# Kernel tuning notes

Hardware: AMD Instinct MI355X
Metric: run time of the kernel (lower is better)

The kernel has to match this reference:

```python
import jax, jax.numpy as jnp
import numpy as np

B, C, OUT, K, H, W = 16, 128, 128, 3, 128, 128
EPS = 1e-5


def setup_inputs() -> dict:
    key = jax.random.key(0)
    ks = jax.random.split(key, 16)
    s = 0.05  # weight init scale to keep activations tame
    d = {
        "ir_feat": jax.random.normal(ks[0], (B, C, H, W), jnp.float32),
        "vi_feat": jax.random.normal(ks[1], (B, C, H, W), jnp.float32),
        # kernel_gen: 1x1 convs on pooled [B,2C,1,1] -> matmuls
        "kg_w1": jax.random.normal(ks[2], (C // 2, 2 * C), jnp.float32) * s,
        "kg_b1": jax.random.normal(ks[3], (C // 2,), jnp.float32) * s,
        "kg_w2": jax.random.normal(ks[4], (OUT * C * K * K, C // 2), jnp.float32) * s,
        "kg_b2": jax.random.normal(ks[5], (OUT * C * K * K,), jnp.float32) * s,
        # bias_gen
        "bg_w1": jax.random.normal(ks[6], (C // 4, 2 * C), jnp.float32) * s,
        "bg_b1": jax.random.normal(ks[7], (C // 4,), jnp.float32) * s,
        "bg_w2": jax.random.normal(ks[8], (OUT, C // 4), jnp.float32) * s,
        "bg_b2": jax.random.normal(ks[9], (OUT,), jnp.float32) * s,
        # enhance: 1x1 conv (no bias) + BN (eval-mode running stats)
        "en_w": jax.random.normal(ks[10], (C, 2 * C), jnp.float32) * s,
        "bn_gamma": jnp.ones((C,), jnp.float32),
        "bn_beta": jnp.zeros((C,), jnp.float32),
        "bn_mean": jax.random.normal(ks[11], (C,), jnp.float32) * 0.1,
        "bn_var": jax.random.uniform(ks[12], (C,), jnp.float32, 0.5, 1.5),
    }
    return d


def reference(ir_feat, vi_feat, kg_w1, kg_b1, kg_w2, kg_b2,
              bg_w1, bg_b1, bg_w2, bg_b2, en_w,
              bn_gamma, bn_beta, bn_mean, bn_var):
    concat = jnp.concatenate([ir_feat, vi_feat], axis=1)        # [B,2C,H,W]
    pooled = concat.mean(axis=(2, 3))                            # AdaptiveAvgPool2d(1) -> [B,2C]

    # dynamic kernel generation (1x1 convs on 1x1 spatial == matmuls)
    hk = jax.nn.relu(pooled @ kg_w1.T + kg_b1)                   # [B,C/2]
    dyn_k = (hk @ kg_w2.T + kg_b2).reshape(B, OUT, C, K, K)      # per-sample conv weights
    hb = jax.nn.relu(pooled @ bg_w1.T + bg_b1)                   # [B,C/4]
    dyn_b = hb @ bg_w2.T + bg_b2                                 # [B,OUT]

    # enhance: 1x1 conv -> BN(eval) -> ReLU
    enh = jnp.einsum('bchw,oc->bohw', concat, en_w)              # [B,C,H,W]
    inv = (bn_gamma / jnp.sqrt(bn_var + EPS))[:, None, None]
    enh = jax.nn.relu(enh * inv + (bn_beta - bn_mean * bn_gamma / jnp.sqrt(bn_var + EPS))[:, None, None])

    # per-sample dynamic conv2d, batched via vmap (replaces the python loop)
    def conv_one(x, w, b):  # x:[C,H,W], w:[OUT,C,K,K], b:[OUT]
        y = jax.lax.conv_general_dilated(
            x[None], w, window_strides=(1, 1), padding=[(1, 1), (1, 1)],
            dimension_numbers=('NCHW', 'OIHW', 'NCHW'))[0]
        return y + b[:, None, None]

    return jax.vmap(conv_one)(enh, dyn_k, dyn_b)                 # [B,OUT,H,W]
```

## Files before the change

### kernel.cpp

```cpp
#include <hip/hip_runtime.h>
#include <hip/hip_bf16.h>

#define B_    16
#define C_    128
#define TWOC  256
#define OUT_  128
#define HW    16384
#define WDIM  128
#define HDIM  128
#define KTOT  1152

typedef __attribute__((ext_vector_type(8))) short short8;
typedef __attribute__((ext_vector_type(4))) float floatx4;

__device__ __forceinline__ ushort f2bf(float f) {
    union { float f; uint u; } x; x.f = f;
    uint r = (x.u + 0x7FFFu + ((x.u >> 16) & 1u)) >> 16;
    return (ushort)r;
}
__device__ __forceinline__ float bf2f(ushort u) {
    union { float f; uint u; } x; x.u = ((uint)u) << 16;
    return x.f;
}
__device__ __forceinline__ uint cvt_pk_bf16(float lo, float hi) {
    uint r;
    asm("v_cvt_pk_bf16_f32 %0, %1, %2" : "=v"(r) : "v"(lo), "v"(hi));
    return r;
}

__global__ __launch_bounds__(256) void prep_kernel(
    const float* __restrict__ en_w, ushort* __restrict__ en_w_bf,
    float* __restrict__ pooled)
{
    int i = blockIdx.x * 256 + threadIdx.x;
    en_w_bf[i] = f2bf(en_w[i]);
    if (i < B_ * TWOC) pooled[i] = 0.f;
}

__global__ __launch_bounds__(256) void enhance_kernel(
    const float* __restrict__ ir, const float* __restrict__ vi,
    const ushort* __restrict__ en_w_bf,
    const float* __restrict__ gamma, const float* __restrict__ beta,
    const float* __restrict__ mean, const float* __restrict__ var,
    ushort* __restrict__ enh, float* __restrict__ pooled)
{
    __shared__ ushort Xs[128][40];
    __shared__ float red[256];
    const int b = blockIdx.y;
    const int p0 = blockIdx.x * 128;
    const int t = threadIdx.x;
    const int lane = t & 63, wave = t >> 6;
    const int wr = wave >> 1, wc = wave & 1;
    const int lr = lane & 15, kg = lane >> 4;
    const int px = t & 127, half = t >> 7;
    const int pc = t & 31, grp = t >> 5;

    floatx4 acc[4][4] = {};
    float fcur[16], fnxt[16];
    short8 a_cur[4], a_nxt[4];

    {
        const float* src = ir + ((size_t)b * C_ + half * 16) * HW + p0 + px;
        #pragma unroll
        for (int jj = 0; jj < 16; ++jj) fcur[jj] = src[(size_t)jj * HW];
        #pragma unroll
        for (int i2 = 0; i2 < 4; ++i2) {
            int co = wr * 64 + i2 * 16 + lr;
            a_cur[i2] = *(const short8*)&en_w_bf[(size_t)co * TWOC + kg * 8];
        }
    }

    #pragma unroll
    for (int kc = 0; kc < 8; ++kc) {
        __syncthreads();
        {
            uint u[8];
            #pragma unroll
            for (int jj = 0; jj < 8; ++jj)
                u[jj] = cvt_pk_bf16(fcur[2 * jj], fcur[2 * jj + 1]);
            uint4* dst = (uint4*)&Xs[px][half * 16];
            dst[0] = make_uint4(u[0], u[1], u[2], u[3]);
            dst[1] = make_uint4(u[4], u[5], u[6], u[7]);
        }
        if (kc > 0 && t < 32) {
            float s = red[t] + red[32 + t] + red[64 + t] + red[96 + t]
                    + red[128 + t] + red[160 + t] + red[192 + t] + red[224 + t];
            atomicAdd(&pooled[b * TWOC + (kc - 1) * 32 + t], s);
        }
        __syncthreads();

        if (kc < 7) {
            int c2b = (kc + 1) * 32 + half * 16;
            const float* src = (c2b < C_)
                ? ir + ((size_t)b * C_ + c2b) * HW + p0 + px
                : vi + ((size_t)b * C_ + (c2b - C_)) * HW + p0 + px;
            #pragma unroll
            for (int jj = 0; jj < 16; ++jj) fnxt[jj] = src[(size_t)jj * HW];
            #pragma unroll
            for (int i2 = 0; i2 < 4; ++i2) {
                int co = wr * 64 + i2 * 16 + lr;
                a_nxt[i2] = *(const short8*)&en_w_bf[(size_t)co * TWOC + (kc + 1) * 32 + kg * 8];
            }
        }

        short8 bfr[4];
        #pragma unroll
        for (int j = 0; j < 4; ++j) {
            int pl = wc * 64 + j * 16 + lr;
            bfr[j] = *(const short8*)&Xs[pl][kg * 8];
        }
        #pragma unroll
        for (int i2 = 0; i2 < 4; ++i2)
            #pragma unroll
            for (int j = 0; j < 4; ++j)
                acc[i2][j] = __builtin_amdgcn_mfma_f32_16x16x32_bf16(a_cur[i2], bfr[j], acc[i2][j], 0, 0, 0);

        {
            float s = 0.f;
            #pragma unroll
            for (int q = 0; q < 16; ++q) s += bf2f(Xs[grp * 16 + q][pc]);
            red[t] = s;
        }

        if (kc < 7) {
            #pragma unroll
            for (int jj = 0; jj < 16; ++jj) fcur[jj] = fnxt[jj];
            #pragma unroll
            for (int i2 = 0; i2 < 4; ++i2) a_cur[i2] = a_nxt[i2];
        }
    }

    __syncthreads();
    if (t < 32) {
        float s = red[t] + red[32 + t] + red[64 + t] + red[96 + t]
                + red[128 + t] + red[160 + t] + red[192 + t] + red[224 + t];
        atomicAdd(&pooled[b * TWOC + 7 * 32 + t], s);
    }

    #pragma unroll
    for (int i2 = 0; i2 < 4; ++i2) {
        int co_b = wr * 64 + i2 * 16 + kg * 4;
        float4 g  = *(const float4*)&gamma[co_b];
        float4 vv = *(const float4*)&var[co_b];
        float4 bt = *(const float4*)&beta[co_b];
        float4 mn = *(const float4*)&mean[co_b];
        float inv0 = g.x * rsqrtf(vv.x + 1e-5f), inv1 = g.y * rsqrtf(vv.y + 1e-5f);
        float inv2 = g.z * rsqrtf(vv.z + 1e-5f), inv3 = g.w * rsqrtf(vv.w + 1e-5f);
        float ad0 = bt.x - mn.x * inv0, ad1 = bt.y - mn.y * inv1;
        float ad2 = bt.z - mn.z * inv2, ad3 = bt.w - mn.w * inv3;
        #pragma unroll
        for (int j = 0; j < 4; ++j) {
            int pl = wc * 64 + j * 16 + lr;
            float v0 = fmaxf(acc[i2][j][0] * inv0 + ad0, 0.f);
            float v1 = fmaxf(acc[i2][j][1] * inv1 + ad1, 0.f);
            float v2 = fmaxf(acc[i2][j][2] * inv2 + ad2, 0.f);
            float v3 = fmaxf(acc[i2][j][3] * inv3 + ad3, 0.f);
            uint2 pk;
            pk.x = cvt_pk_bf16(v0, v1);
            pk.y = cvt_pk_bf16(v2, v3);
            *(uint2*)&enh[((size_t)b * HW + p0 + pl) * C_ + co_b] = pk;
        }
    }
}

__global__ __launch_bounds__(256) void gen_mlp1_kernel(
    const float* __restrict__ pooled,
    const float* __restrict__ kg_w1, const float* __restrict__ kg_b1,
    const float* __restrict__ bg_w1, const float* __restrict__ bg_b1,
    float* __restrict__ hk, float* __restrict__ hb)
{
    const float scale = 1.0f / (float)HW;
    int idx = blockIdx.x * 256 + threadIdx.x;
    if (idx < B_ * 64) {
        int b = idx >> 6, j = idx & 63;
        const float4* w = (const float4*)(kg_w1 + (size_t)j * TWOC);
        const float4* p = (const float4*)(pooled + b * TWOC);
        float s = 0.f;
        #pragma unroll 8
        for (int q = 0; q < 64; ++q) {
            float4 wv = w[q], pv = p[q];
            s += (wv.x * pv.x + wv.y * pv.y) + (wv.z * pv.z + wv.w * pv.w);
        }
        hk[idx] = fmaxf(kg_b1[j] + s * scale, 0.f);
    } else if (idx < B_ * 64 + B_ * 32) {
        int e = idx - B_ * 64;
        int b = e >> 5, j = e & 31;
        const float4* w = (const float4*)(bg_w1 + (size_t)j * TWOC);
        const float4* p = (const float4*)(pooled + b * TWOC);
        float s = 0.f;
        #pragma unroll 8
        for (int q = 0; q < 64; ++q) {
            float4 wv = w[q], pv = p[q];
            s += (wv.x * pv.x + wv.y * pv.y) + (wv.z * pv.z + wv.w * pv.w);
        }
        hb[e] = fmaxf(bg_b1[j] + s * scale, 0.f);
    }
}

__global__ __launch_bounds__(256) void gen_dynk_kernel(
    const float* __restrict__ kg_w2, const float* __restrict__ kg_b2,
    const float* __restrict__ hk, const float* __restrict__ hb,
    const float* __restrict__ bg_w2, const float* __restrict__ bg_b2,
    ushort* __restrict__ dynk, float* __restrict__ dyn_b)
{
    __shared__ float hk_s[B_][64];
    int t = threadIdx.x;
    for (int i = t; i < B_ * 64; i += 256) hk_s[i >> 6][i & 63] = hk[i];
    __syncthreads();

    int i = blockIdx.x * 256 + t;
    int kk = i >> 14;
    int o  = (i >> 7) & 127;
    int c  = i & 127;
    int r  = o * KTOT + c * 9 + kk;

    float wrow[64];
    const float4* w4 = (const float4*)(kg_w2 + (size_t)r * 64);
    #pragma unroll
    for (int q = 0; q < 16; ++q) {
        float4 v = w4[q];
        wrow[4 * q + 0] = v.x; wrow[4 * q + 1] = v.y;
        wrow[4 * q + 2] = v.z; wrow[4 * q + 3] = v.w;
    }
    float bias = kg_b2[r];
    #pragma unroll
    for (int b = 0; b < B_; ++b) {
        float s = bias;
        #pragma unroll
        for (int k2 = 0; k2 < 64; ++k2) s += hk_s[b][k2] * wrow[k2];
        dynk[((size_t)(b * 9 + kk) * 128 + o) * 128 + c] = f2bf(s);
    }

    if (blockIdx.x == 0) {
        for (int e = t; e < B_ * OUT_; e += 256) {
            int b = e >> 7, o2 = e & 127;
            float s = bg_b2[o2];
            const float* w = bg_w2 + o2 * 32;
            const float* h = hb + b * 32;
            #pragma unroll
            for (int k2 = 0; k2 < 32; ++k2) s += h[k2] * w[k2];
            dyn_b[e] = s;
        }
    }
}

#define TY_   4
#define TX_   32
#define HX_   34
#define NPX_  204

__global__ __launch_bounds__(256, 4) void dynconv_kernel(
    const ushort* __restrict__ enh, const ushort* __restrict__ dynk,
    const float* __restrict__ dyn_b, float* __restrict__ out)
{
    __shared__ ushort halo[NPX_][72];
    const int pid = blockIdx.x;
    const int lid = (pid & 7) * 512 + (pid >> 3);
    const int b   = lid >> 8;
    const int rem = lid & 255;
    const int oh  = rem & 1;
    const int tile = rem >> 1;
    const int ty = tile >> 2, tx = tile & 3;
    const int gy0 = ty * TY_, gx0 = tx * TX_;

    const int t = threadIdx.x, lane = t & 63, wc = t >> 6;
    const int lr = lane & 15, kg = lane >> 4;
    const ushort* dynk_b = dynk + (size_t)b * 9 * 128 * 128;
    const ushort* enh_b  = enh + (size_t)b * HW * C_;

    floatx4 acc[4][2] = {};
    short8 a_cur[8], a_nxt[8];

    for (int h = 0; h < 2; ++h) {
        uint4 hreg[7];
        #pragma unroll
        for (int s = 0; s < 7; ++s) {
            int seg = s * 256 + t;
            int hp = seg >> 3, c8 = seg & 7;
            uint4 v = make_uint4(0, 0, 0, 0);
            if (hp < NPX_) {
                int hy = hp / HX_, hx = hp - hy * HX_;
                int gy = gy0 - 1 + hy, gx = gx0 - 1 + hx;
                if ((unsigned)gy < 128u && (unsigned)gx < 128u)
                    v = *(const uint4*)&enh_b[((size_t)(gy * WDIM + gx)) * C_ + h * 64 + c8 * 8];
            }
            hreg[s] = v;
        }
        #pragma unroll
        for (int q = 0; q < 8; ++q) {
            int ks = q >> 2, i2 = q & 3;
            int o = oh * 64 + i2 * 16 + lr;
            a_cur[q] = *(const short8*)&dynk_b[(size_t)(0 * 128 + o) * 128 + h * 64 + ks * 32 + kg * 8];
        }
        __syncthreads();
        #pragma unroll
        for (int s = 0; s < 7; ++s) {
            int seg = s * 256 + t;
            int hp = seg >> 3, c8 = seg & 7;
            if (hp < NPX_) *(uint4*)&halo[hp][c8 * 8] = hreg[s];
        }
        __syncthreads();

        #pragma unroll
        for (int kk = 0; kk < 9; ++kk) {
            if (kk < 8) {
                #pragma unroll
                for (int q = 0; q < 8; ++q) {
                    int ks = q >> 2, i2 = q & 3;
                    int o = oh * 64 + i2 * 16 + lr;
                    a_nxt[q] = *(const short8*)&dynk_b[(size_t)((kk + 1) * 128 + o) * 128 + h * 64 + ks * 32 + kg * 8];
                }
            }
            const int kh = kk / 3, kw = kk - kh * 3;
            #pragma unroll
            for (int ks = 0; ks < 2; ++ks) {
                short8 bfr[2];
                #pragma unroll
                for (int j = 0; j < 2; ++j)
                    bfr[j] = *(const short8*)&halo[(wc + kh) * HX_ + j * 16 + lr + kw][ks * 32 + kg * 8];
                #pragma unroll
                for (int i2 = 0; i2 < 4; ++i2)
                    #pragma unroll
                    for (int j = 0; j < 2; ++j)
                        acc[i2][j] = __builtin_amdgcn_mfma_f32_16x16x32_bf16(a_cur[ks * 4 + i2], bfr[j], acc[i2][j], 0, 0, 0);
            }
            #pragma unroll
            for (int q = 0; q < 8; ++q) a_cur[q] = a_nxt[q];
        }
    }

    const int gy = gy0 + wc;
    #pragma unroll
    for (int i2 = 0; i2 < 4; ++i2) {
        int o_b = oh * 64 + i2 * 16 + kg * 4;
        float4 db = *(const float4*)&dyn_b[b * OUT_ + o_b];
        float dbv[4] = {db.x, db.y, db.z, db.w};
        #pragma unroll
        for (int j = 0; j < 2; ++j) {
            int gx = gx0 + j * 16 + lr;
            #pragma unroll
            for (int r = 0; r < 4; ++r) {
                int o = o_b + r;
                out[((size_t)(b * OUT_ + o)) * HW + gy * WDIM + gx] = acc[i2][j][r] + dbv[r];
            }
        }
    }
}

extern "C" void kernel_launch(void* const* d_in, const int* in_sizes, int n_in,
                              void* d_out, int out_size, void* d_ws, size_t ws_size,
                              hipStream_t stream)
{
    const float* ir    = (const float*)d_in[0];
    const float* vi    = (const float*)d_in[1];
    const float* kg_w1 = (const float*)d_in[2];
    const float* kg_b1 = (const float*)d_in[3];
    const float* kg_w2 = (const float*)d_in[4];
    const float* kg_b2 = (const float*)d_in[5];
    const float* bg_w1 = (const float*)d_in[6];
    const float* bg_b1 = (const float*)d_in[7];
    const float* bg_w2 = (const float*)d_in[8];
    const float* bg_b2 = (const float*)d_in[9];
    const float* en_w  = (const float*)d_in[10];
    const float* bn_g  = (const float*)d_in[11];
    const float* bn_b  = (const float*)d_in[12];
    const float* bn_m  = (const float*)d_in[13];
    const float* bn_v  = (const float*)d_in[14];
    float* out = (float*)d_out;

    char* ws = (char*)d_ws;
    float*  pooled = (float*)(ws + 0);
    float*  dyn_b  = (float*)(ws + 16384);
    float*  hk     = (float*)(ws + 24576);
    float*  hb     = (float*)(ws + 28672);
    ushort* dynk   = (ushort*)(ws + 32768);
    ushort* enh    = (ushort*)(ws + 32768 + 4718592);

    size_t en_off = 32768 + 4718592 + 67108864;
    ushort* en_w_bf = (ws_size >= en_off + 65536)
                    ? (ushort*)(ws + en_off)
                    : (ushort*)((char*)d_out + (size_t)out_size - 65536);

    prep_kernel<<<128, 256, 0, stream>>>(en_w, en_w_bf, pooled);
    enhance_kernel<<<dim3(HDIM, B_), 256, 0, stream>>>(ir, vi, en_w_bf, bn_g, bn_b,
                                                       bn_m, bn_v, enh, pooled);
    gen_mlp1_kernel<<<6, 256, 0, stream>>>(pooled, kg_w1, kg_b1, bg_w1, bg_b1, hk, hb);
    gen_dynk_kernel<<<576, 256, 0, stream>>>(kg_w2, kg_b2, hk, hb, bg_w2, bg_b2, dynk, dyn_b);
    dynconv_kernel<<<4096, 256, 0, stream>>>(enh, dynk, dyn_b, out);
}
```

Before: 664.8 us.

## Cover all output channels per block in dynconv with a 2x2 wave tiling

```diff
diff --git a/kernel.cpp b/kernel.cpp
--- a/kernel.cpp
+++ b/kernel.cpp
@@ -255,21 +255,19 @@
 {
     __shared__ ushort halo[NPX_][72];
     const int pid = blockIdx.x;
-    const int lid = (pid & 7) * 512 + (pid >> 3);
-    const int b   = lid >> 8;
-    const int rem = lid & 255;
-    const int oh  = rem & 1;
-    const int tile = rem >> 1;
-    const int ty = tile >> 2, tx = tile & 3;
+    const int lid = (pid & 7) * 256 + (pid >> 3);
+    const int b   = lid >> 7;
+    const int rem = lid & 127;
+    const int ty = rem >> 2, tx = rem & 3;
     const int gy0 = ty * TY_, gx0 = tx * TX_;
 
-    const int t = threadIdx.x, lane = t & 63, wc = t >> 6;
+    const int t = threadIdx.x, lane = t & 63, wave = t >> 6;
+    const int wr = wave >> 1, wc = wave & 1;
     const int lr = lane & 15, kg = lane >> 4;
     const ushort* dynk_b = dynk + (size_t)b * 9 * 128 * 128;
     const ushort* enh_b  = enh + (size_t)b * HW * C_;
 
-    floatx4 acc[4][2] = {};
-    short8 a_cur[8], a_nxt[8];
+    floatx4 acc[4][4] = {};
 
     for (int h = 0; h < 2; ++h) {
         uint4 hreg[7];
@@ -286,12 +284,6 @@
             }
             hreg[s] = v;
         }
-        #pragma unroll
-        for (int q = 0; q < 8; ++q) {
-            int ks = q >> 2, i2 = q & 3;
-            int o = oh * 64 + i2 * 16 + lr;
-            a_cur[q] = *(const short8*)&dynk_b[(size_t)(0 * 128 + o) * 128 + h * 64 + ks * 32 + kg * 8];
-        }
         __syncthreads();
         #pragma unroll
         for (int s = 0; s < 7; ++s) {
@@ -303,41 +295,40 @@
 
         #pragma unroll
         for (int kk = 0; kk < 9; ++kk) {
-            if (kk < 8) {
+            const int kh = kk / 3, kw = kk - kh * 3;
+            #pragma unroll
+            for (int ks = 0; ks < 2; ++ks) {
+                short8 a[4], bfr[4];
                 #pragma unroll
-                for (int q = 0; q < 8; ++q) {
-                    int ks = q >> 2, i2 = q & 3;
-                    int o = oh * 64 + i2 * 16 + lr;
-                    a_nxt[q] = *(const short8*)&dynk_b[(size_t)((kk + 1) * 128 + o) * 128 + h * 64 + ks * 32 + kg * 8];
+                for (int i2 = 0; i2 < 4; ++i2) {
+                    int o = wr * 64 + i2 * 16 + lr;
+                    a[i2] = *(const short8*)&dynk_b[(size_t)(kk * 128 + o) * 128 + h * 64 + ks * 32 + kg * 8];
                 }
-            }
-            const int kh = kk / 3, kw = kk - kh * 3;
-            #pragma unroll
-            for (int ks = 0; ks < 2; ++ks) {
-                short8 bfr[2];
                 #pragma unroll
-                for (int j = 0; j < 2; ++j)
-                    bfr[j] = *(const short8*)&halo[(wc + kh) * HX_ + j * 16 + lr + kw][ks * 32 + kg * 8];
+                for (int j = 0; j < 4; ++j) {
+                    int p = wc * 64 + j * 16 + lr;
+                    int py = p >> 5, pxc = p & 31;
+                    bfr[j] = *(const short8*)&halo[(py + kh) * HX_ + pxc + kw][ks * 32 + kg * 8];
+                }
                 #pragma unroll
                 for (int i2 = 0; i2 < 4; ++i2)
                     #pragma unroll
-                    for (int j = 0; j < 2; ++j)
-                        acc[i2][j] = __builtin_amdgcn_mfma_f32_16x16x32_bf16(a_cur[ks * 4 + i2], bfr[j], acc[i2][j], 0, 0, 0);
+                    for (int j = 0; j < 4; ++j)
+                        acc[i2][j] = __builtin_amdgcn_mfma_f32_16x16x32_bf16(a[i2], bfr[j], acc[i2][j], 0, 0, 0);
             }
-            #pragma unroll
-            for (int q = 0; q < 8; ++q) a_cur[q] = a_nxt[q];
-        }
-    }
-
-    const int gy = gy0 + wc;
+        }
+    }
+
     #pragma unroll
     for (int i2 = 0; i2 < 4; ++i2) {
-        int o_b = oh * 64 + i2 * 16 + kg * 4;
+        int o_b = wr * 64 + i2 * 16 + kg * 4;
         float4 db = *(const float4*)&dyn_b[b * OUT_ + o_b];
         float dbv[4] = {db.x, db.y, db.z, db.w};
         #pragma unroll
-        for (int j = 0; j < 2; ++j) {
-            int gx = gx0 + j * 16 + lr;
+        for (int j = 0; j < 4; ++j) {
+            int p = wc * 64 + j * 16 + lr;
+            int py = p >> 5, pxc = p & 31;
+            int gy = gy0 + py, gx = gx0 + pxc;
             #pragma unroll
             for (int r = 0; r < 4; ++r) {
                 int o = o_b + r;
@@ -386,5 +377,5 @@
                                                        bn_m, bn_v, enh, pooled);
     gen_mlp1_kernel<<<6, 256, 0, stream>>>(pooled, kg_w1, kg_b1, bg_w1, bg_b1, hk, hb);
     gen_dynk_kernel<<<576, 256, 0, stream>>>(kg_w2, kg_b2, hk, hb, bg_w2, bg_b2, dynk, dyn_b);
-    dynconv_kernel<<<4096, 256, 0, stream>>>(enh, dynk, dyn_b, out);
-}
+    dynconv_kernel<<<2048, 256, 0, stream>>>(enh, dynk, dyn_b, out);
+}
```

Result: faster. 591.5 us (-11.0%).
